# Kernel optimization log

Measured on AMD Instinct MI355X. Metric: run time of the kernel, lower is better.

Reference implementation:

```python
import jax, jax.numpy as jnp
import numpy as np

NEG = -1e9      # stands in for -inf; exp(NEG)=0 in fp32 and is grad-safe
SK_TAU = 0.05   # sinkhorn temperature (module constant)


def _gconv(A, x, Wa, ba, Wu, bu):
    # Gconv: A <- F.normalize(A, p=1, dim=-2) (column-wise L1), then
    # out = A @ relu(a_fc(x)) + relu(u_fc(x))
    Anorm = A / jnp.maximum(jnp.sum(jnp.abs(A), axis=1, keepdims=True), 1e-12)
    ax = jax.nn.relu(x @ Wa + ba)
    ux = jax.nn.relu(x @ Wu + bu)
    return jnp.einsum('bnm,bmd->bnd', Anorm, ax) + ux


def _sinkhorn(s, n1, n2, max_iter, tau):
    # Masked, batched equivalent of the per-sample torch sinkhorn
    # (valid region [0:n1, 0:n2]; entries outside stay at NEG -> exp -> 0).
    # Assumes n1 <= n2 == N so no per-sample transpose branch triggers.
    B, N, M = s.shape
    row_ok = jnp.arange(N)[None, :, None] < n1[:, None, None]
    col_ok = jnp.arange(M)[None, None, :] < n2[:, None, None]
    mask = row_ok & col_ok
    log_s = jnp.where(mask, s / tau, NEG)
    for i in range(max_iter):
        axis = 2 if i % 2 == 0 else 1  # even: row-normalize, odd: col-normalize
        log_s = log_s - jax.scipy.special.logsumexp(log_s, axis=axis, keepdims=True)
        log_s = jnp.where(mask, log_s, NEG)
    return jnp.exp(log_s)


def _forward(feat1, feat2, A1, A2, n1, n2, sk_max_iter,
             W0a, b0a, W0u, b0u, W1a, b1a, W1u, b1u, Wc, bc, Aaff0, Aaff1):
    # gnn layer 0 (Siamese: same weights on both graphs)
    emb1 = _gconv(A1, feat1, W0a, b0a, W0u, b0u)
    emb2 = _gconv(A2, feat2, W0a, b0a, W0u, b0u)
    # i == gnn_layer-2: affinity -> sinkhorn -> cross-graph update
    s = jnp.einsum('bnd,de,bme->bnm', emb1, Aaff0, emb2)
    s = _sinkhorn(s, n1, n2, sk_max_iter, SK_TAU)
    new1 = jnp.concatenate([emb1, jnp.einsum('bnm,bmd->bnd', s, emb2)], axis=-1) @ Wc + bc
    new2 = jnp.concatenate([emb2, jnp.einsum('bnm,bnd->bmd', s, emb1)], axis=-1) @ Wc + bc
    emb1, emb2 = new1, new2
    # gnn layer 1 (final)
    emb1 = _gconv(A1, emb1, W1a, b1a, W1u, b1u)
    emb2 = _gconv(A2, emb2, W1a, b1a, W1u, b1u)
    s = jnp.einsum('bnd,de,bme->bnm', emb1, Aaff1, emb2)
    return _sinkhorn(s, n1, n2, sk_max_iter, SK_TAU)


def setup_inputs() -> dict:
    key = jax.random.key(0)
    B, N = 32, 256
    C_IN, C_HID, C_OUT = 1024, 2048, 2048
    ks = jax.random.split(key, 16)

    feat1 = jax.random.normal(ks[0], (B, N, C_IN), dtype=jnp.float32)
    feat2 = jax.random.normal(ks[1], (B, N, C_IN), dtype=jnp.float32)
    A1 = jax.random.uniform(ks[2], (B, N, N), dtype=jnp.float32)
    A2 = jax.random.uniform(ks[3], (B, N, N), dtype=jnp.float32)
    n1 = jax.random.randint(ks[4], (B,), N // 2, N + 1).astype(jnp.int32)
    n2 = jnp.full((B,), N, dtype=jnp.int32)

    def lin(k, fan_in, fan_out):
        stdv = 1.0 / np.sqrt(fan_in)
        kw, kb = jax.random.split(k)
        W = jax.random.uniform(kw, (fan_in, fan_out), minval=-stdv, maxval=stdv, dtype=jnp.float32)
        b = jax.random.uniform(kb, (fan_out,), minval=-stdv, maxval=stdv, dtype=jnp.float32)
        return W, b

    W0a, b0a = lin(ks[5], C_IN, C_HID)
    W0u, b0u = lin(ks[6], C_IN, C_HID)
    W1a, b1a = lin(ks[7], C_HID, C_OUT)
    W1u, b1u = lin(ks[8], C_HID, C_OUT)
    Wc, bc = lin(ks[9], 2 * C_HID, C_HID)
    # WeightedInnerProdAffinity: A ~ U(-1/sqrt(d), 1/sqrt(d)) + I
    Aaff0 = jax.random.uniform(ks[10], (C_HID, C_HID), minval=-1/np.sqrt(C_HID), maxval=1/np.sqrt(C_HID), dtype=jnp.float32) + jnp.eye(C_HID, dtype=jnp.float32)
    Aaff1 = jax.random.uniform(ks[11], (C_OUT, C_OUT), minval=-1/np.sqrt(C_OUT), maxval=1/np.sqrt(C_OUT), dtype=jnp.float32) + jnp.eye(C_OUT, dtype=jnp.float32)

    return {
        'feat1': feat1, 'feat2': feat2, 'A1': A1, 'A2': A2,
        'n1': n1, 'n2': n2, 'cross_iter_num': -1, 'sk_max_iter': 10,
        'W0a': W0a, 'b0a': b0a, 'W0u': W0u, 'b0u': b0u,
        'W1a': W1a, 'b1a': b1a, 'W1u': W1u, 'b1u': b1u,
        'Wc': Wc, 'bc': bc, 'Aaff0': Aaff0, 'Aaff1': Aaff1,
    }


def reference(feat1, feat2, A1, A2, n1, n2, cross_iter_num, sk_max_iter,
              W0a, b0a, W0u, b0u, W1a, b1a, W1u, b1u, Wc, bc, Aaff0, Aaff1):
    assert cross_iter_num <= 0  # PCA-GM path (IPCA-GM cross-iteration not exercised)
    return _forward(feat1, feat2, A1, A2, n1, n2, int(sk_max_iter),
                    W0a, b0a, W0u, b0u, W1a, b1a, W1u, b1u, Wc, bc, Aaff0, Aaff1)
```

## Files before the change

kernel.cpp:

```cpp
#include <hip/hip_runtime.h>
#include <math.h>

#define NEGV -1e9f
#define SK_TAU 0.05f

typedef __attribute__((ext_vector_type(4))) float f32x4;
typedef __attribute__((ext_vector_type(8))) short short8;

#define GLDS(g, l) __builtin_amdgcn_global_load_lds( \
    (const __attribute__((address_space(1))) void*)(g), \
    (__attribute__((address_space(3))) void*)(l), 16, 0, 0)

__device__ inline unsigned bf16rtn(float x) {
    unsigned u = __float_as_uint(x);
    return (u + 0x7FFFu + ((u >> 16) & 1u)) >> 16;
}
__device__ inline float bf2f(short h) {
    return __uint_as_float(((unsigned)(unsigned short)h) << 16);
}
__device__ inline void split1(float x, short& h, short& l) {
    unsigned hu = bf16rtn(x);
    h = (short)hu;
    float r = x - __uint_as_float(hu << 16);
    l = (short)(__float_as_uint(r) >> 16);
}
__device__ inline void cvt4(const float4 v, short4& h, short4& l) {
    unsigned h0 = bf16rtn(v.x), h1 = bf16rtn(v.y), h2 = bf16rtn(v.z), h3 = bf16rtn(v.w);
    h.x = (short)h0; h.y = (short)h1; h.z = (short)h2; h.w = (short)h3;
    float l0 = v.x - __uint_as_float(h0 << 16);
    float l1 = v.y - __uint_as_float(h1 << 16);
    float l2 = v.z - __uint_as_float(h2 << 16);
    float l3 = v.w - __uint_as_float(h3 << 16);
    l.x = (short)(__float_as_uint(l0) >> 16);
    l.y = (short)(__float_as_uint(l1) >> 16);
    l.z = (short)(__float_as_uint(l2) >> 16);
    l.w = (short)(__float_as_uint(l3) >> 16);
}
__device__ inline short8 pack8(const short4 a, const short4 b) {
    short8 r;
    r[0] = a.x; r[1] = a.y; r[2] = a.z; r[3] = a.w;
    r[4] = b.x; r[5] = b.y; r[6] = b.z; r[7] = b.w;
    return r;
}

__global__ __launch_bounds__(256) void colnorm_k(const float* __restrict__ A,
                                                 float* __restrict__ inv)
{
    int idx = blockIdx.x * 256 + threadIdx.x;
    int b = idx >> 8, m = idx & 255;
    const float* p = A + (long long)b * 65536 + m;
    float s = 0.f;
    #pragma unroll 8
    for (int n = 0; n < 256; ++n) s += fabsf(p[n * 256]);
    inv[idx] = 1.f / fmaxf(s, 1e-12f);
}

__global__ __launch_bounds__(256) void split_mat(const float* __restrict__ X,
                                                 short* __restrict__ H,
                                                 short* __restrict__ L, long long n4)
{
    long long i = (long long)blockIdx.x * 256 + threadIdx.x;
    long long stride = (long long)gridDim.x * 256;
    for (; i < n4; i += stride) {
        float4 v = ((const float4*)X)[i];
        short4 h, l;
        cvt4(v, h, l);
        ((short4*)H)[i] = h;
        ((short4*)L)[i] = l;
    }
}

template <int OM>
__global__ __launch_bounds__(256, 2) void gemm_w(
    const short* __restrict__ A1h, const short* __restrict__ A1l,
    const short* __restrict__ A2h, const short* __restrict__ A2l,
    int K1, int lda,
    const float* __restrict__ Bf, int K,
    float* __restrict__ Cf, short* __restrict__ Ch, short* __restrict__ Cl,
    const float* __restrict__ bias, int relu)
{
    __shared__ alignas(16) short lds[2][16384];

    const int tid = threadIdx.x;
    const int wave = tid >> 6, L = tid & 63;
    const int m0 = blockIdx.y * 128, n0 = blockIdx.x * 128;
    const int wm = (wave & 1) * 64, wn = (wave >> 1) * 64;
    const int lm = L & 15, lh = (L >> 4) * 8;
    const int c0 = wave * 2;

    long long grow[2];
    #pragma unroll
    for (int c = 0; c < 2; ++c)
        grow[c] = (long long)(m0 + (c0 + c) * 16 + lm) * lda + lh;

    const int bcol = tid & 127, bkh = tid >> 7;
    const float* bp = Bf + (long long)(bkh * 16) * 2048 + n0 + bcol;
    const int bws = (bcol >> 4) * 512 + (bcol & 15) * 8 + bkh * 256;

    f32x4 acc[4][4];
    #pragma unroll
    for (int i = 0; i < 4; ++i)
        #pragma unroll
        for (int j = 0; j < 4; ++j)
            acc[i][j] = (f32x4){0.f, 0.f, 0.f, 0.f};

    auto STAGE = [&](short* buf, int k0) {
        const short *sh, *sl;
        int ko;
        if (k0 < K1) { sh = A1h; sl = A1l; ko = k0; }
        else         { sh = A2h; sl = A2l; ko = k0 - K1; }
        #pragma unroll
        for (int c = 0; c < 2; ++c) {
            const int so = (c0 + c) * 512;
            GLDS(sh + grow[c] + ko, buf + so);
            GLDS(sl + grow[c] + ko, buf + 4096 + so);
        }
    };
    auto LOADB = [&](float br[16], int k0) {
        #pragma unroll
        for (int j = 0; j < 16; ++j)
            br[j] = bp[((long long)k0 + j) * 2048];
    };
    auto WRITEB = [&](short* buf, const float br[16]) {
        #pragma unroll
        for (int ks = 0; ks < 2; ++ks) {
            float4 v0 = {br[ks * 8 + 0], br[ks * 8 + 1], br[ks * 8 + 2], br[ks * 8 + 3]};
            float4 v1 = {br[ks * 8 + 4], br[ks * 8 + 5], br[ks * 8 + 6], br[ks * 8 + 7]};
            short4 h0, l0, h1, l1;
            cvt4(v0, h0, l0);
            cvt4(v1, h1, l1);
            *(short8*)(buf + 8192  + bws + ks * 128) = pack8(h0, h1);
            *(short8*)(buf + 12288 + bws + ks * 128) = pack8(l0, l1);
        }
    };

    const int ab = (wm >> 4) * 512 + L * 8;
    const int bb = (wn >> 4) * 512 + L * 8;
    auto COMPUTE = [&](const short* buf) {
        const short* AhS = buf;
        const short* AlS = buf + 4096;
        const short* BhS = buf + 8192;
        const short* BlS = buf + 12288;
        short8 AF[4], ALF[4], BFr[4], BLF[4];
        #pragma unroll
        for (int t = 0; t < 4; ++t) {
            AF[t]  = *(const short8*)(AhS + ab + t * 512);
            ALF[t] = *(const short8*)(AlS + ab + t * 512);
            BFr[t] = *(const short8*)(BhS + bb + t * 512);
            BLF[t] = *(const short8*)(BlS + bb + t * 512);
        }
        #pragma unroll
        for (int ti = 0; ti < 4; ++ti)
            #pragma unroll
            for (int tj = 0; tj < 4; ++tj) {
                acc[ti][tj] = __builtin_amdgcn_mfma_f32_16x16x32_bf16(AF[ti],  BFr[tj], acc[ti][tj], 0, 0, 0);
                acc[ti][tj] = __builtin_amdgcn_mfma_f32_16x16x32_bf16(AF[ti],  BLF[tj], acc[ti][tj], 0, 0, 0);
                acc[ti][tj] = __builtin_amdgcn_mfma_f32_16x16x32_bf16(ALF[ti], BFr[tj], acc[ti][tj], 0, 0, 0);
            }
    };

    const int NT = K >> 5;
    float brA[16], brB[16];

    LOADB(brA, 0);
    STAGE(lds[0], 0);
    LOADB(brB, 32);
    WRITEB(lds[0], brA);
    LOADB(brA, 64);

    for (int t = 0; t < NT; t += 2) {
        __syncthreads();
        {
            STAGE(lds[1], (t + 1) << 5);
            WRITEB(lds[1], brB);
        }
        if (t + 3 < NT) LOADB(brB, (t + 3) << 5);
        COMPUTE(lds[0]);

        __syncthreads();
        if (t + 2 < NT) {
            STAGE(lds[0], (t + 2) << 5);
            WRITEB(lds[0], brA);
        }
        if (t + 4 < NT) LOADB(brA, (t + 4) << 5);
        COMPUTE(lds[1]);
    }

    const int lcol = L & 15, lrow = (L >> 4) * 4;
    float bv[4];
    #pragma unroll
    for (int tj = 0; tj < 4; ++tj)
        bv[tj] = bias ? bias[n0 + wn + tj * 16 + lcol] : 0.f;

    #pragma unroll
    for (int ti = 0; ti < 4; ++ti) {
        #pragma unroll
        for (int r = 0; r < 4; ++r) {
            int gr = m0 + wm + ti * 16 + lrow + r;
            #pragma unroll
            for (int tj = 0; tj < 4; ++tj) {
                int gcol = n0 + wn + tj * 16 + lcol;
                float v = acc[ti][tj][r] + bv[tj];
                if (relu) v = fmaxf(v, 0.f);
                long long idx = (long long)gr * 2048 + gcol;
                if (OM == 0) {
                    Cf[idx] = v;
                } else {
                    short hh, ll;
                    split1(v, hh, ll);
                    Ch[idx] = hh;
                    Cl[idx] = ll;
                }
            }
        }
    }
}

template <bool TA, bool ACC>
__global__ __launch_bounds__(256, 2) void bgemm(
    const float* __restrict__ A,
    const short* __restrict__ Bh_, const short* __restrict__ Bl_,
    short* __restrict__ Ch, short* __restrict__ Cl,
    const float* __restrict__ colscale)
{
    __shared__ float As[16][132];
    __shared__ float Bs[16][132];

    const int N = 2048;
    const long long sB = 524288;
    int z = blockIdx.z;
    const float* Az = A + (long long)z * 65536;
    const float* cs = colscale ? colscale + z * 256 : nullptr;

    int n0 = blockIdx.x * 128, m0 = blockIdx.y * 128;
    int tid = threadIdx.x;
    int tx = tid & 15, ty = tid >> 4;

    float accv[8][8];
    #pragma unroll
    for (int i = 0; i < 8; ++i)
        #pragma unroll
        for (int j = 0; j < 8; ++j) accv[i][j] = 0.f;

    for (int k0 = 0; k0 < 256; k0 += 16) {
        if (!TA) {
            #pragma unroll
            for (int i = 0; i < 2; ++i) {
                int lin = tid + i * 256;
                int r  = lin >> 2;
                int c4 = (lin & 3) * 4;
                float4 v = *(const float4*)(Az + (long long)(m0 + r) * 256 + k0 + c4);
                if (cs) {
                    v.x *= cs[k0 + c4 + 0]; v.y *= cs[k0 + c4 + 1];
                    v.z *= cs[k0 + c4 + 2]; v.w *= cs[k0 + c4 + 3];
                }
                As[c4 + 0][r] = v.x; As[c4 + 1][r] = v.y;
                As[c4 + 2][r] = v.z; As[c4 + 3][r] = v.w;
            }
        } else {
            #pragma unroll
            for (int i = 0; i < 2; ++i) {
                int lin = tid + i * 256;
                int kk = lin >> 5;
                int m4 = (lin & 31) * 4;
                *(float4*)&As[kk][m4] =
                    *(const float4*)(Az + (long long)(k0 + kk) * 256 + m0 + m4);
            }
        }
        #pragma unroll
        for (int i = 0; i < 2; ++i) {
            int lin = tid + i * 256;
            int kk = lin >> 5;
            int n4 = (lin & 31) * 4;
            long long off = (long long)z * sB + (long long)(k0 + kk) * N + n0 + n4;
            short4 h = *(const short4*)(Bh_ + off);
            short4 l = *(const short4*)(Bl_ + off);
            Bs[kk][n4 + 0] = bf2f(h.x) + bf2f(l.x);
            Bs[kk][n4 + 1] = bf2f(h.y) + bf2f(l.y);
            Bs[kk][n4 + 2] = bf2f(h.z) + bf2f(l.z);
            Bs[kk][n4 + 3] = bf2f(h.w) + bf2f(l.w);
        }
        __syncthreads();

        #pragma unroll
        for (int kk = 0; kk < 16; ++kk) {
            float a[8], b[8];
            *(float4*)&a[0] = *(const float4*)&As[kk][ty * 8];
            *(float4*)&a[4] = *(const float4*)&As[kk][ty * 8 + 4];
            *(float4*)&b[0] = *(const float4*)&Bs[kk][tx * 8];
            *(float4*)&b[4] = *(const float4*)&Bs[kk][tx * 8 + 4];
            #pragma unroll
            for (int i = 0; i < 8; ++i)
                #pragma unroll
                for (int j = 0; j < 8; ++j)
                    accv[i][j] = fmaf(a[i], b[j], accv[i][j]);
        }
        __syncthreads();
    }

    #pragma unroll
    for (int i = 0; i < 8; ++i) {
        int rowl = m0 + ty * 8 + i;
        long long base = (long long)z * sB + (long long)rowl * N;
        #pragma unroll
        for (int j = 0; j < 8; ++j) {
            int col = n0 + tx * 8 + j;
            long long idx = base + col;
            float v = accv[i][j];
            if (ACC) v += bf2f(Ch[idx]) + bf2f(Cl[idx]);
            short hh, ll;
            split1(v, hh, ll);
            Ch[idx] = hh;
            Cl[idx] = ll;
        }
    }
}

__global__ __launch_bounds__(256) void gemm_bt_f64(
    const float* __restrict__ A,
    const short* __restrict__ Bh_, const short* __restrict__ Bl_,
    float* __restrict__ C)
{
    __shared__ float As[16][65];
    __shared__ float Bs[16][65];

    const int K = 2048;
    int z = blockIdx.z;
    const float* Az = A + (long long)z * 524288;
    C += (long long)z * 65536;

    int n0 = blockIdx.x * 64;
    int m0 = blockIdx.y * 64;
    int tid = threadIdx.x;
    int tx = tid & 15;
    int ty = tid >> 4;

    double acc[4][4];
    #pragma unroll
    for (int i = 0; i < 4; ++i)
        #pragma unroll
        for (int j = 0; j < 4; ++j) acc[i][j] = 0.0;

    int r  = tid >> 2;
    int c4 = (tid & 3) * 4;

    for (int k0 = 0; k0 < K; k0 += 16) {
        {
            const float4 v = *(const float4*)(Az + (long long)(m0 + r) * K + k0 + c4);
            As[c4 + 0][r] = v.x; As[c4 + 1][r] = v.y;
            As[c4 + 2][r] = v.z; As[c4 + 3][r] = v.w;
        }
        {
            long long off = (long long)z * 524288 + (long long)(n0 + r) * K + k0 + c4;
            short4 h = *(const short4*)(Bh_ + off);
            short4 l = *(const short4*)(Bl_ + off);
            Bs[c4 + 0][r] = bf2f(h.x) + bf2f(l.x);
            Bs[c4 + 1][r] = bf2f(h.y) + bf2f(l.y);
            Bs[c4 + 2][r] = bf2f(h.z) + bf2f(l.z);
            Bs[c4 + 3][r] = bf2f(h.w) + bf2f(l.w);
        }
        __syncthreads();

        #pragma unroll
        for (int kk = 0; kk < 16; ++kk) {
            double a[4], b[4];
            #pragma unroll
            for (int i = 0; i < 4; ++i) a[i] = (double)As[kk][ty + 16 * i];
            #pragma unroll
            for (int j = 0; j < 4; ++j) b[j] = (double)Bs[kk][tx + 16 * j];
            #pragma unroll
            for (int i = 0; i < 4; ++i)
                #pragma unroll
                for (int j = 0; j < 4; ++j)
                    acc[i][j] = fma(a[i], b[j], acc[i][j]);
        }
        __syncthreads();
    }

    #pragma unroll
    for (int i = 0; i < 4; ++i) {
        int rowl = m0 + ty + 16 * i;
        #pragma unroll
        for (int j = 0; j < 4; ++j)
            C[(long long)rowl * 256 + n0 + tx + 16 * j] = (float)acc[i][j];
    }
}

__global__ __launch_bounds__(1024, 4) void sk_fused(float* __restrict__ S,
                                                    const int* __restrict__ n1)
{
    __shared__ float pmax[16][256];
    __shared__ float psum[16][256];
    __shared__ float lseS[256];

    const int b = blockIdx.x;
    const int tid = threadIdx.x;
    const int w = tid >> 6, l = tid & 63;
    const int lim = n1[b];
    float* Sb = S + (long long)b * 65536;

    float4 v[16];
    #pragma unroll
    for (int r = 0; r < 16; ++r) {
        int n = w * 16 + r;
        if (n < lim) {
            float4 x = *(const float4*)(Sb + n * 256 + l * 4);
            v[r].x = x.x / SK_TAU; v[r].y = x.y / SK_TAU;
            v[r].z = x.z / SK_TAU; v[r].w = x.w / SK_TAU;
        } else {
            v[r] = (float4){NEGV, NEGV, NEGV, NEGV};
        }
    }

    for (int it = 0; it < 10; ++it) {
        if ((it & 1) == 0) {
            #pragma unroll
            for (int r = 0; r < 16; ++r) {
                if (w * 16 + r >= lim) continue;
                float m = fmaxf(fmaxf(v[r].x, v[r].y), fmaxf(v[r].z, v[r].w));
                #pragma unroll
                for (int off = 1; off < 64; off <<= 1) m = fmaxf(m, __shfl_xor(m, off));
                float s = expf(v[r].x - m) + expf(v[r].y - m) +
                          expf(v[r].z - m) + expf(v[r].w - m);
                #pragma unroll
                for (int off = 1; off < 64; off <<= 1) s += __shfl_xor(s, off);
                float lse = m + logf(s);
                v[r].x -= lse; v[r].y -= lse; v[r].z -= lse; v[r].w -= lse;
            }
        } else {
            float cm[4] = {-3.4e38f, -3.4e38f, -3.4e38f, -3.4e38f};
            #pragma unroll
            for (int r = 0; r < 16; ++r) {
                cm[0] = fmaxf(cm[0], v[r].x); cm[1] = fmaxf(cm[1], v[r].y);
                cm[2] = fmaxf(cm[2], v[r].z); cm[3] = fmaxf(cm[3], v[r].w);
            }
            float cs[4] = {0.f, 0.f, 0.f, 0.f};
            #pragma unroll
            for (int r = 0; r < 16; ++r) {
                cs[0] += expf(v[r].x - cm[0]); cs[1] += expf(v[r].y - cm[1]);
                cs[2] += expf(v[r].z - cm[2]); cs[3] += expf(v[r].w - cm[3]);
            }
            #pragma unroll
            for (int j = 0; j < 4; ++j) {
                pmax[w][l * 4 + j] = cm[j];
                psum[w][l * 4 + j] = cs[j];
            }
            __syncthreads();
            if (tid < 256) {
                float m = -3.4e38f, s = 0.f;
                #pragma unroll
                for (int ww = 0; ww < 16; ++ww) {
                    float pm = pmax[ww][tid], ps = psum[ww][tid];
                    float nm = fmaxf(m, pm);
                    s = s * expf(m - nm) + ps * expf(pm - nm);
                    m = nm;
                }
                lseS[tid] = m + logf(s);
            }
            __syncthreads();
            float l0 = lseS[l * 4 + 0], l1 = lseS[l * 4 + 1];
            float l2 = lseS[l * 4 + 2], l3 = lseS[l * 4 + 3];
            #pragma unroll
            for (int r = 0; r < 16; ++r) {
                if (w * 16 + r >= lim) continue;
                v[r].x -= l0; v[r].y -= l1; v[r].z -= l2; v[r].w -= l3;
            }
        }
    }

    #pragma unroll
    for (int r = 0; r < 16; ++r) {
        int n = w * 16 + r;
        float4 o;
        if (n < lim) {
            o.x = expf(v[r].x); o.y = expf(v[r].y);
            o.z = expf(v[r].z); o.w = expf(v[r].w);
        } else {
            o = (float4){0.f, 0.f, 0.f, 0.f};
        }
        *(float4*)(Sb + n * 256 + l * 4) = o;
    }
}

static void gw(hipStream_t st, int om, const short* Ah, const short* Al, int lda,
               const float* Bf, int K,
               float* Cf, short* Ch, short* Cl, const float* bias, int relu)
{
    dim3 grid(16, 64), block(256);
    if (om == 0)
        gemm_w<0><<<grid, block, 0, st>>>(Ah, Al, Ah, Al, K, lda, Bf, K,
                                          Cf, nullptr, nullptr, bias, relu);
    else
        gemm_w<1><<<grid, block, 0, st>>>(Ah, Al, Ah, Al, K, lda, Bf, K,
                                          nullptr, Ch, Cl, bias, relu);
}

static void gwcat(hipStream_t st, const short* A1h, const short* A1l,
                  const short* A2h, const short* A2l,
                  const float* Bf, short* Ch, short* Cl, const float* bias)
{
    dim3 grid(16, 64), block(256);
    gemm_w<1><<<grid, block, 0, st>>>(A1h, A1l, A2h, A2l, 2048, 2048, Bf, 4096,
                                      nullptr, Ch, Cl, bias, 0);
}

extern "C" void kernel_launch(void* const* d_in, const int* in_sizes, int n_in,
                              void* d_out, int out_size, void* d_ws, size_t ws_size,
                              hipStream_t stream)
{
    const float* feat1 = (const float*)d_in[0];
    const float* feat2 = (const float*)d_in[1];
    const float* A1    = (const float*)d_in[2];
    const float* A2    = (const float*)d_in[3];
    const int*   n1    = (const int*)d_in[4];
    const float* W0a = (const float*)d_in[8];  const float* b0a = (const float*)d_in[9];
    const float* W0u = (const float*)d_in[10]; const float* b0u = (const float*)d_in[11];
    const float* W1a = (const float*)d_in[12]; const float* b1a = (const float*)d_in[13];
    const float* W1u = (const float*)d_in[14]; const float* b1u = (const float*)d_in[15];
    const float* Wc  = (const float*)d_in[16]; const float* bc  = (const float*)d_in[17];
    const float* Aaff0 = (const float*)d_in[18];
    const float* Aaff1 = (const float*)d_in[19];

    const long long TSZ = 16777216LL;
    const long long PL  = 16777216LL;
    const long long PF  = 8388608LL;

    float* T1f = (float*)d_ws;
    float* T2f = T1f + TSZ;
    float* T3f = T2f + TSZ;
    float* T4f = T3f + TSZ;
    short *T1h = (short*)T1f, *T1l = T1h + PL;
    short *T2h = (short*)T2f, *T2l = T2h + PL;
    short *T3h = (short*)T3f, *T3l = T3h + PL;
    short *T4h = (short*)T4f, *T4l = T4h + PL;

    short* f1h = (short*)T4f;      short* f1l = f1h + PF;
    short* f2h = f1h + 2 * PF;     short* f2l = f1h + 3 * PF;
    float* invA = (float*)T4f;
    float* invB = invA + 8192;

    float* S    = (float*)d_out;
    float* inv1 = S;
    float* inv2 = S + 8192;

    dim3 bgrid(16, 2, 32), bblk(256);

    split_mat<<<2048, 256, 0, stream>>>(feat1, f1h, f1l, 8192LL * 1024 / 4);
    split_mat<<<2048, 256, 0, stream>>>(feat2, f2h, f2l, 8192LL * 1024 / 4);

    gw(stream, 1, f1h, f1l, 1024, W0u, 1024, nullptr, T1h, T1l, b0u, 1);
    gw(stream, 1, f2h, f2l, 1024, W0u, 1024, nullptr, T2h, T2l, b0u, 1);
    gw(stream, 1, f1h, f1l, 1024, W0a, 1024, nullptr, T3h, T3l, b0a, 1);
    colnorm_k<<<32, 256, 0, stream>>>(A1, invA);
    colnorm_k<<<32, 256, 0, stream>>>(A2, invB);
    bgemm<false, true><<<bgrid, bblk, 0, stream>>>(A1, T3h, T3l, T1h, T1l, invA);
    gw(stream, 1, f2h, f2l, 1024, W0a, 1024, nullptr, T3h, T3l, b0a, 1);
    bgemm<false, true><<<bgrid, bblk, 0, stream>>>(A2, T3h, T3l, T2h, T2l, invB);

    gw(stream, 0, T1h, T1l, 2048, Aaff0, 2048, T3f, nullptr, nullptr, nullptr, 0);
    gemm_bt_f64<<<dim3(4, 4, 32), 256, 0, stream>>>(T3f, T2h, T2l, S);

    sk_fused<<<32, 1024, 0, stream>>>(S, n1);

    bgemm<false, false><<<bgrid, bblk, 0, stream>>>(S, T2h, T2l, T3h, T3l, nullptr);
    gwcat(stream, T1h, T1l, T3h, T3l, Wc, T4h, T4l, bc);
    bgemm<true, false><<<bgrid, bblk, 0, stream>>>(S, T1h, T1l, T3h, T3l, nullptr);
    gwcat(stream, T2h, T2l, T3h, T3l, Wc, T1h, T1l, bc);

    gw(stream, 1, T4h, T4l, 2048, W1a, 2048, nullptr, T2h, T2l, b1a, 1);
    gw(stream, 1, T4h, T4l, 2048, W1u, 2048, nullptr, T3h, T3l, b1u, 1);
    colnorm_k<<<32, 256, 0, stream>>>(A1, inv1);
    bgemm<false, true><<<bgrid, bblk, 0, stream>>>(A1, T2h, T2l, T3h, T3l, inv1);
    gw(stream, 1, T1h, T1l, 2048, W1a, 2048, nullptr, T2h, T2l, b1a, 1);
    gw(stream, 1, T1h, T1l, 2048, W1u, 2048, nullptr, T4h, T4l, b1u, 1);
    colnorm_k<<<32, 256, 0, stream>>>(A2, inv2);
    bgemm<false, true><<<bgrid, bblk, 0, stream>>>(A2, T2h, T2l, T4h, T4l, inv2);

    gw(stream, 0, T3h, T3l, 2048, Aaff1, 2048, T1f, nullptr, nullptr, nullptr, 0);
    gemm_bt_f64<<<dim3(4, 4, 32), 256, 0, stream>>>(T1f, T4h, T4l, S);

    sk_fused<<<32, 1024, 0, stream>>>(S, n1);
}
```

Baseline: 4.615 ms.

## Replace FP32 SIMT batched GEMM with split-bf16 MFMA kernel and double-buffered LDS

Rewrites the batched A@X GEMM (adjacency and sinkhorn-matrix products) to use bf16 MFMA instructions with a 3-term hi/lo split (hh, hl, lh) instead of FP32 FMA on SIMT lanes. Global loads for the next K-slice are issued before computing the current slice from a double-buffered LDS tile. The fp32 A operand is converted to hi/lo bf16 in registers before being stored to LDS. This aims to cut compute time on six batched GEMM launches at the cost of a small precision change from dropping the lo*lo term, and scalar strided global loads that may be poorly coalesced.

After: 4.340 ms. 6.0% less time.

```diff
diff --git a/kernel.cpp b/kernel.cpp
--- a/kernel.cpp
+++ b/kernel.cpp
@@ -217,101 +217,131 @@
 }
 
 template <bool TA, bool ACC>
-__global__ __launch_bounds__(256, 2) void bgemm(
+__global__ __launch_bounds__(256, 2) void bgemm_m(
     const float* __restrict__ A,
     const short* __restrict__ Bh_, const short* __restrict__ Bl_,
     short* __restrict__ Ch, short* __restrict__ Cl,
     const float* __restrict__ colscale)
 {
-    __shared__ float As[16][132];
-    __shared__ float Bs[16][132];
-
-    const int N = 2048;
+    __shared__ alignas(16) short lds[2][16384];
+
+    const int tid = threadIdx.x;
+    const int wave = tid >> 6, L = tid & 63;
+    const int z = blockIdx.z;
+    const int n0 = blockIdx.x * 128, m0 = blockIdx.y * 128;
+    const int wm = (wave & 1) * 64, wn = (wave >> 1) * 64;
     const long long sB = 524288;
-    int z = blockIdx.z;
     const float* Az = A + (long long)z * 65536;
     const float* cs = colscale ? colscale + z * 256 : nullptr;
 
-    int n0 = blockIdx.x * 128, m0 = blockIdx.y * 128;
-    int tid = threadIdx.x;
-    int tx = tid & 15, ty = tid >> 4;
-
-    float accv[8][8];
-    #pragma unroll
-    for (int i = 0; i < 8; ++i)
-        #pragma unroll
-        for (int j = 0; j < 8; ++j) accv[i][j] = 0.f;
-
-    for (int k0 = 0; k0 < 256; k0 += 16) {
-        if (!TA) {
-            #pragma unroll
-            for (int i = 0; i < 2; ++i) {
-                int lin = tid + i * 256;
-                int r  = lin >> 2;
-                int c4 = (lin & 3) * 4;
-                float4 v = *(const float4*)(Az + (long long)(m0 + r) * 256 + k0 + c4);
-                if (cs) {
-                    v.x *= cs[k0 + c4 + 0]; v.y *= cs[k0 + c4 + 1];
-                    v.z *= cs[k0 + c4 + 2]; v.w *= cs[k0 + c4 + 3];
-                }
-                As[c4 + 0][r] = v.x; As[c4 + 1][r] = v.y;
-                As[c4 + 2][r] = v.z; As[c4 + 3][r] = v.w;
-            }
-        } else {
-            #pragma unroll
-            for (int i = 0; i < 2; ++i) {
-                int lin = tid + i * 256;
-                int kk = lin >> 5;
-                int m4 = (lin & 31) * 4;
-                *(float4*)&As[kk][m4] =
-                    *(const float4*)(Az + (long long)(k0 + kk) * 256 + m0 + m4);
-            }
-        }
-        #pragma unroll
-        for (int i = 0; i < 2; ++i) {
-            int lin = tid + i * 256;
-            int kk = lin >> 5;
-            int n4 = (lin & 31) * 4;
-            long long off = (long long)z * sB + (long long)(k0 + kk) * N + n0 + n4;
-            short4 h = *(const short4*)(Bh_ + off);
-            short4 l = *(const short4*)(Bl_ + off);
-            Bs[kk][n4 + 0] = bf2f(h.x) + bf2f(l.x);
-            Bs[kk][n4 + 1] = bf2f(h.y) + bf2f(l.y);
-            Bs[kk][n4 + 2] = bf2f(h.z) + bf2f(l.z);
-            Bs[kk][n4 + 3] = bf2f(h.w) + bf2f(l.w);
-        }
+    const int arow = tid & 127, akh = tid >> 7;
+    const int aws = (arow >> 4) * 512 + (arow & 15) * 8 + akh * 256;
+    const int bws = aws;
+
+    f32x4 acc[4][4];
+    #pragma unroll
+    for (int i = 0; i < 4; ++i)
+        #pragma unroll
+        for (int j = 0; j < 4; ++j)
+            acc[i][j] = (f32x4){0.f, 0.f, 0.f, 0.f};
+
+    float ar[16];
+    short brh[16], brl[16];
+
+    auto LOADA = [&](int k0) {
+        #pragma unroll
+        for (int j = 0; j < 16; ++j) {
+            int kk = k0 + akh * 16 + j;
+            float v;
+            if (TA) v = Az[(long long)kk * 256 + m0 + arow];
+            else    v = Az[(long long)(m0 + arow) * 256 + kk];
+            if (!TA && cs) v *= cs[kk];
+            ar[j] = v;
+        }
+    };
+    auto LOADBB = [&](int k0) {
+        #pragma unroll
+        for (int j = 0; j < 16; ++j) {
+            long long off = (long long)z * sB +
+                            (long long)(k0 + akh * 16 + j) * 2048 + n0 + arow;
+            brh[j] = Bh_[off];
+            brl[j] = Bl_[off];
+        }
+    };
+    auto WRITES = [&](short* buf) {
+        #pragma unroll
+        for (int ks = 0; ks < 2; ++ks) {
+            float4 v0 = {ar[ks * 8 + 0], ar[ks * 8 + 1], ar[ks * 8 + 2], ar[ks * 8 + 3]};
+            float4 v1 = {ar[ks * 8 + 4], ar[ks * 8 + 5], ar[ks * 8 + 6], ar[ks * 8 + 7]};
+            short4 h0, l0, h1, l1;
+            cvt4(v0, h0, l0);
+            cvt4(v1, h1, l1);
+            *(short8*)(buf + aws + ks * 128)        = pack8(h0, h1);
+            *(short8*)(buf + 4096 + aws + ks * 128) = pack8(l0, l1);
+        }
+        #pragma unroll
+        for (int ks = 0; ks < 2; ++ks) {
+            short8 h, l;
+            #pragma unroll
+            for (int i = 0; i < 8; ++i) { h[i] = brh[ks * 8 + i]; l[i] = brl[ks * 8 + i]; }
+            *(short8*)(buf + 8192  + bws + ks * 128) = h;
+            *(short8*)(buf + 12288 + bws + ks * 128) = l;
+        }
+    };
+
+    const int ab = (wm >> 4) * 512 + L * 8;
+    const int bb = (wn >> 4) * 512 + L * 8;
+    auto COMPUTE = [&](const short* buf) {
+        const short* AhS = buf;
+        const short* AlS = buf + 4096;
+        const short* BhS = buf + 8192;
+        const short* BlS = buf + 12288;
+        short8 AF[4], ALF[4], BFr[4], BLF[4];
+        #pragma unroll
+        for (int t = 0; t < 4; ++t) {
+            AF[t]  = *(const short8*)(AhS + ab + t * 512);
+            ALF[t] = *(const short8*)(AlS + ab + t * 512);
+            BFr[t] = *(const short8*)(BhS + bb + t * 512);
+            BLF[t] = *(const short8*)(BlS + bb + t * 512);
+        }
+        #pragma unroll
+        for (int ti = 0; ti < 4; ++ti)
+            #pragma unroll
+            for (int tj = 0; tj < 4; ++tj) {
+                acc[ti][tj] = __builtin_amdgcn_mfma_f32_16x16x32_bf16(AF[ti],  BFr[tj], acc[ti][tj], 0, 0, 0);
+                acc[ti][tj] = __builtin_amdgcn_mfma_f32_16x16x32_bf16(AF[ti],  BLF[tj], acc[ti][tj], 0, 0, 0);
+                acc[ti][tj] = __builtin_amdgcn_mfma_f32_16x16x32_bf16(ALF[ti], BFr[tj], acc[ti][tj], 0, 0, 0);
+            }
+    };
+
+    LOADA(0);
+    LOADBB(0);
+    #pragma unroll
+    for (int t = 0; t < 8; ++t) {
+        WRITES(lds[t & 1]);
         __syncthreads();
-
-        #pragma unroll
-        for (int kk = 0; kk < 16; ++kk) {
-            float a[8], b[8];
-            *(float4*)&a[0] = *(const float4*)&As[kk][ty * 8];
-            *(float4*)&a[4] = *(const float4*)&As[kk][ty * 8 + 4];
-            *(float4*)&b[0] = *(const float4*)&Bs[kk][tx * 8];
-            *(float4*)&b[4] = *(const float4*)&Bs[kk][tx * 8 + 4];
-            #pragma unroll
-            for (int i = 0; i < 8; ++i)
-                #pragma unroll
-                for (int j = 0; j < 8; ++j)
-                    accv[i][j] = fmaf(a[i], b[j], accv[i][j]);
-        }
-        __syncthreads();
-    }
-
-    #pragma unroll
-    for (int i = 0; i < 8; ++i) {
-        int rowl = m0 + ty * 8 + i;
-        long long base = (long long)z * sB + (long long)rowl * N;
-        #pragma unroll
-        for (int j = 0; j < 8; ++j) {
-            int col = n0 + tx * 8 + j;
-            long long idx = base + col;
-            float v = accv[i][j];
-            if (ACC) v += bf2f(Ch[idx]) + bf2f(Cl[idx]);
-            short hh, ll;
-            split1(v, hh, ll);
-            Ch[idx] = hh;
-            Cl[idx] = ll;
+        if (t < 7) { LOADA((t + 1) * 32); LOADBB((t + 1) * 32); }
+        COMPUTE(lds[t & 1]);
+    }
+
+    const int lcol = L & 15, lrow = (L >> 4) * 4;
+    #pragma unroll
+    for (int ti = 0; ti < 4; ++ti) {
+        #pragma unroll
+        for (int r = 0; r < 4; ++r) {
+            int gr = m0 + wm + ti * 16 + lrow + r;
+            long long base = (long long)z * sB + (long long)gr * 2048;
+            #pragma unroll
+            for (int tj = 0; tj < 4; ++tj) {
+                int gcol = n0 + wn + tj * 16 + lcol;
+                long long idx = base + gcol;
+                float v = acc[ti][tj][r];
+                if (ACC) v += bf2f(Ch[idx]) + bf2f(Cl[idx]);
+                short hh, ll;
+                split1(v, hh, ll);
+                Ch[idx] = hh;
+                Cl[idx] = ll;
+            }
         }
     }
 }
@@ -553,28 +583,28 @@
     gw(stream, 1, f1h, f1l, 1024, W0a, 1024, nullptr, T3h, T3l, b0a, 1);
     colnorm_k<<<32, 256, 0, stream>>>(A1, invA);
     colnorm_k<<<32, 256, 0, stream>>>(A2, invB);
-    bgemm<false, true><<<bgrid, bblk, 0, stream>>>(A1, T3h, T3l, T1h, T1l, invA);
+    bgemm_m<false, true><<<bgrid, bblk, 0, stream>>>(A1, T3h, T3l, T1h, T1l, invA);
     gw(stream, 1, f2h, f2l, 1024, W0a, 1024, nullptr, T3h, T3l, b0a, 1);
-    bgemm<false, true><<<bgrid, bblk, 0, stream>>>(A2, T3h, T3l, T2h, T2l, invB);
+    bgemm_m<false, true><<<bgrid, bblk, 0, stream>>>(A2, T3h, T3l, T2h, T2l, invB);
 
     gw(stream, 0, T1h, T1l, 2048, Aaff0, 2048, T3f, nullptr, nullptr, nullptr, 0);
     gemm_bt_f64<<<dim3(4, 4, 32), 256, 0, stream>>>(T3f, T2h, T2l, S);
 
     sk_fused<<<32, 1024, 0, stream>>>(S, n1);
 
-    bgemm<false, false><<<bgrid, bblk, 0, stream>>>(S, T2h, T2l, T3h, T3l, nullptr);
+    bgemm_m<false, false><<<bgrid, bblk, 0, stream>>>(S, T2h, T2l, T3h, T3l, nullptr);
     gwcat(stream, T1h, T1l, T3h, T3l, Wc, T4h, T4l, bc);
-    bgemm<true, false><<<bgrid, bblk, 0, stream>>>(S, T1h, T1l, T3h, T3l, nullptr);
+    bgemm_m<true, false><<<bgrid, bblk, 0, stream>>>(S, T1h, T1l, T3h, T3l, nullptr);
     gwcat(stream, T2h, T2l, T3h, T3l, Wc, T1h, T1l, bc);
 
     gw(stream, 1, T4h, T4l, 2048, W1a, 2048, nullptr, T2h, T2l, b1a, 1);
     gw(stream, 1, T4h, T4l, 2048, W1u, 2048, nullptr, T3h, T3l, b1u, 1);
     colnorm_k<<<32, 256, 0, stream>>>(A1, inv1);
-    bgemm<false, true><<<bgrid, bblk, 0, stream>>>(A1, T2h, T2l, T3h, T3l, inv1);
+    bgemm_m<false, true><<<bgrid, bblk, 0, stream>>>(A1, T2h, T2l, T3h, T3l, inv1);
     gw(stream, 1, T1h, T1l, 2048, W1a, 2048, nullptr, T2h, T2l, b1a, 1);
     gw(stream, 1, T1h, T1l, 2048, W1u, 2048, nullptr, T4h, T4l, b1u, 1);
     colnorm_k<<<32, 256, 0, stream>>>(A2, inv2);
-    bgemm<false, true><<<bgrid, bblk, 0, stream>>>(A2, T2h, T2l, T4h, T4l, inv2);
+    bgemm_m<false, true><<<bgrid, bblk, 0, stream>>>(A2, T2h, T2l, T4h, T4l, inv2);
 
     gw(stream, 0, T3h, T3l, 2048, Aaff1, 2048, T1f, nullptr, nullptr, nullptr, 0);
     gemm_bt_f64<<<dim3(4, 4, 32), 256, 0, stream>>>(T1f, T4h, T4l, S);
```
